# Optimization experiments

Measured on AMD Instinct MI355X. Metric: run time of the kernel, lower is better.

Reference implementation:

```python
import jax, jax.numpy as jnp
import numpy as np

B, S, E, H = 4, 2048, 768, 12
D = E // H  # head dimension = 64


def setup_inputs() -> dict:
    key = jax.random.key(0)
    ks = jax.random.split(key, 10)
    scale = 1.0 / np.sqrt(E)
    x = jax.random.normal(ks[0], (B, S, E), dtype=jnp.float32)
    mask = jax.random.randint(ks[1], (B, S), 0, 2, dtype=jnp.int32)
    # per-head Q/K/V projections stacked over heads: [H, E, D]
    Wq = jax.random.normal(ks[2], (H, E, D), dtype=jnp.float32) * scale
    bq = jax.random.normal(ks[3], (H, D), dtype=jnp.float32) * scale
    Wk = jax.random.normal(ks[4], (H, E, D), dtype=jnp.float32) * scale
    bk = jax.random.normal(ks[5], (H, D), dtype=jnp.float32) * scale
    Wv = jax.random.normal(ks[6], (H, E, D), dtype=jnp.float32) * scale
    bv = jax.random.normal(ks[7], (H, D), dtype=jnp.float32) * scale
    # output projection: [H*D, E]
    Wo = jax.random.normal(ks[8], (H * D, E), dtype=jnp.float32) * scale
    bo = jax.random.normal(ks[9], (E,), dtype=jnp.float32) * scale
    return {"x": x, "mask": mask, "Wq": Wq, "bq": bq, "Wk": Wk, "bk": bk,
            "Wv": Wv, "bv": bv, "Wo": Wo, "bo": bo}


def reference(x, mask, Wq, bq, Wk, bk, Wv, bv, Wo, bo):
    # Per-head linear projections, vectorized over heads: [B, H, S, D]
    q = jnp.einsum('bse,hed->bhsd', x, Wq) + bq[None, :, None, :]
    k = jnp.einsum('bse,hed->bhsd', x, Wk) + bk[None, :, None, :]
    v = jnp.einsum('bse,hed->bhsd', x, Wv) + bv[None, :, None, :]
    # scores: [B, H, S, S]
    scores = jnp.einsum('bhqd,bhkd->bhqk', q, k) / jnp.sqrt(jnp.float32(D))
    # mask [B, S] broadcast over heads and query positions (key-side mask)
    key_mask = mask[:, None, None, :]  # [B, 1, 1, S]
    scores = jnp.where(key_mask == 0, jnp.float32(-1e9), scores)
    attn = jax.nn.softmax(scores, axis=-1)
    out = jnp.einsum('bhqk,bhkd->bhqd', attn, v)  # [B, H, S, D]
    # concat heads: [B, S, H*D]
    out = out.transpose(0, 2, 1, 3).reshape(B, S, H * D)
    return out @ Wo + bo
```

## Files before the change

### kernel.cpp

```cpp
#include <hip/hip_runtime.h>
#include <hip/hip_bf16.h>

#define B_ 4
#define S_ 2048
#define E_ 768
#define H_ 12
#define D_ 64
#define M_ (B_*S_)
#define NQKV 2304
#define KDIM 768

typedef __bf16 bf16x8 __attribute__((ext_vector_type(8)));
typedef float f32x4 __attribute__((ext_vector_type(4)));
typedef short shortx4 __attribute__((ext_vector_type(4)));
typedef unsigned int uintx2 __attribute__((ext_vector_type(2)));
typedef unsigned int uintx4 __attribute__((ext_vector_type(4)));

typedef __attribute__((address_space(1))) void gvoid;
typedef __attribute__((address_space(3))) void lvoid;

__device__ __forceinline__ void gl_lds16(const void* g, void* l) {
  __builtin_amdgcn_global_load_lds((gvoid*)g, (lvoid*)l, 16, 0, 0);
}

__device__ __forceinline__ f32x4 mfma16(bf16x8 a, bf16x8 b, f32x4 c) {
  return __builtin_amdgcn_mfma_f32_16x16x32_bf16(a, b, c, 0, 0, 0);
}

__device__ __forceinline__ f32x4 mfma_pv(shortx4 a, shortx4 b, f32x4 c) {
#if __has_builtin(__builtin_amdgcn_mfma_f32_16x16x16bf16_1k)
  return __builtin_amdgcn_mfma_f32_16x16x16bf16_1k(a, b, c, 0, 0, 0);
#else
  uintx2 au = __builtin_bit_cast(uintx2, a);
  uintx2 bu = __builtin_bit_cast(uintx2, b);
  uintx4 aw = {au.x, au.y, 0u, 0u};
  uintx4 bw = {bu.x, bu.y, 0u, 0u};
  return mfma16(__builtin_bit_cast(bf16x8, aw), __builtin_bit_cast(bf16x8, bw), c);
#endif
}

__device__ __forceinline__ __bf16 ldmix(const void* p, size_t idx, int is_bf) {
  if (is_bf) return ((const __bf16*)p)[idx];
  return (__bf16)(((const float*)p)[idx]);
}
__device__ __forceinline__ float ldmixf(const void* p, size_t idx, int is_bf) {
  if (is_bf) return (float)((const __bf16*)p)[idx];
  return ((const float*)p)[idx];
}

__global__ __launch_bounds__(256) void detect_scan_kernel(
    const unsigned short* __restrict__ xr, int* __restrict__ flag,
    const int* __restrict__ mask,
    int* __restrict__ R, float* __restrict__ maskC, int* __restrict__ npadArr)
{
  __shared__ int cnt;
  __shared__ int wtot[4];
  __shared__ int runningS;
  const int t = threadIdx.x;
  if (blockIdx.x == 0) {
    if (t == 0) cnt = 0;
    __syncthreads();
    unsigned short h = xr[2 * t];
    int e = (h >> 7) & 0xFF;
    if (e >= 100 && e <= 140) atomicAdd(&cnt, 1);
    __syncthreads();
    if (t == 0) *flag = (cnt > 148) ? 1 : 0;
    return;
  }
  const int w = t >> 6, lane = t & 63;
  const int b = blockIdx.x - 1;
  if (t == 0) runningS = 0;
  __syncthreads();
  for (int k0 = 0; k0 < S_; k0 += 256) {
    int keep = (mask[b * S_ + k0 + t] != 0) ? 1 : 0;
    unsigned long long bal = __ballot(keep);
    int lanePre = __popcll(bal & ((1ull << lane) - 1ull));
    if (lane == 0) wtot[w] = __popcll(bal);
    __syncthreads();
    int base = runningS;
    for (int i = 0; i < w; ++i) base += wtot[i];
    if (keep) {
      int pos = base + lanePre;
      R[b * S_ + pos] = b * S_ + k0 + t;
      maskC[b * S_ + pos] = 0.f;
    }
    __syncthreads();
    if (t == 0) runningS += wtot[0] + wtot[1] + wtot[2] + wtot[3];
    __syncthreads();
  }
  int n = runningS;
  int np = (n + 63) & ~63;
  for (int j = n + t; j < S_; j += 256) {
    R[b * S_ + j] = b * S_;
    maskC[b * S_ + j] = -1.0e9f;
  }
  if (t == 0) npadArr[b] = np;
}

__global__ __launch_bounds__(256) void prep_kernel(
    const void* __restrict__ x,
    const void* __restrict__ Wq, const void* __restrict__ bq,
    const void* __restrict__ Wk, const void* __restrict__ bk,
    const void* __restrict__ Wv, const void* __restrict__ bv,
    const void* __restrict__ Wo, const void* __restrict__ bo,
    const int* __restrict__ flag,
    __bf16* __restrict__ Xb,
    __bf16* __restrict__ WbT, __bf16* __restrict__ WoT,
    float* __restrict__ biasP, float* __restrict__ biasO)
{
  const int is_bf = *flag;
  const int bid = blockIdx.x;
  const int t = threadIdx.x;
  if (bid < 3072) {
    int base = (bid * 256 + t) * 8;
    if (is_bf) {
      *(uintx4*)(Xb + base) = *(const uintx4*)((const __bf16*)x + base);
    } else {
      const float* xf = (const float*)x + base;
      f32x4 a = *(const f32x4*)xf;
      f32x4 c = *(const f32x4*)(xf + 4);
      __bf16 ov[8] = {(__bf16)a[0], (__bf16)a[1], (__bf16)a[2], (__bf16)a[3],
                      (__bf16)c[0], (__bf16)c[1], (__bf16)c[2], (__bf16)c[3]};
      *(uintx4*)(Xb + base) = *(uintx4*)ov;
    }
    return;
  }
  int idx = (bid - 3072) * 256 + t;
  const int NW = NQKV * KDIM;
  if (idx < NW) {
    int n = idx / KDIM;
    int e = idx - n * KDIM;
    int sel = n / 768;
    int hd  = n - sel * 768;
    int h = hd >> 6, d = hd & 63;
    const void* W = (sel == 0) ? Wq : (sel == 1) ? Wk : Wv;
    WbT[idx] = ldmix(W, (size_t)(h * 768 + e) * 64 + d, is_bf);
  } else {
    int idx2 = idx - NW;
    int n = idx2 / 768;
    int k = idx2 - n * 768;
    WoT[idx2] = ldmix(Wo, (size_t)k * 768 + n, is_bf);
  }
  if (idx < NQKV) {
    int sel = idx / 768;
    int hd = idx - sel * 768;
    const void* bsel = (sel == 0) ? bq : (sel == 1) ? bk : bv;
    biasP[idx] = ldmixf(bsel, hd, is_bf);
  }
  if (idx >= NW && idx < NW + 768) {
    biasO[idx - NW] = ldmixf(bo, idx - NW, is_bf);
  }
}

__global__ __launch_bounds__(256) void gemm_qkv(
    const __bf16* __restrict__ Xb,
    const __bf16* __restrict__ WbT,
    const float* __restrict__ biasP,
    const int* __restrict__ R,
    const int* __restrict__ npadArr,
    __bf16* __restrict__ Qc,
    __bf16* __restrict__ Kc,
    __bf16* __restrict__ Vc)
{
  __shared__ __align__(16) __bf16 As[128 * 32];
  __shared__ __align__(16) __bf16 Bs[64 * 32];
  const int t = threadIdx.x;
  const int wave = t >> 6, lane = t & 63;
  const int l15 = lane & 15, lq = lane >> 4;
  const int wm = (wave & 1) * 64;
  const int wn = (wave >> 1) * 32;

  const int bid = blockIdx.x;
  int m0, bn0, isQ, b = 0;
  int rowA0, rowA1;
  if (bid < 768) {
    isQ = 1;
    int mi = bid / 12, ni = bid - mi * 12;
    m0 = mi * 128; bn0 = ni * 64;
    rowA0 = m0 + ((0 * 256 + t) >> 2);
    rowA1 = m0 + ((1 * 256 + t) >> 2);
  } else {
    isQ = 0;
    int r2 = bid - 768;
    b = r2 / 384;
    int rr = r2 - b * 384;
    int mi = rr / 24, ni = rr - mi * 24;
    if (mi * 128 >= npadArr[b]) return;
    m0 = mi * 128;
    bn0 = 768 + ni * 64;
    rowA0 = R[b * S_ + m0 + ((0 * 256 + t) >> 2)];
    rowA1 = R[b * S_ + m0 + ((1 * 256 + t) >> 2)];
  }
  const int c8 = (t & 3) << 3;
  const int brow = t >> 2;

  const f32x4 z4 = {0.f, 0.f, 0.f, 0.f};
  f32x4 acc[4][2];
#pragma unroll
  for (int i = 0; i < 4; ++i)
#pragma unroll
    for (int j = 0; j < 2; ++j) acc[i][j] = z4;

  for (int k0 = 0; k0 < KDIM; k0 += 32) {
    __syncthreads();
    gl_lds16(Xb + (size_t)rowA0 * KDIM + k0 + c8, As + (size_t)(wave * 64) * 8);
    gl_lds16(Xb + (size_t)rowA1 * KDIM + k0 + c8, As + (size_t)(256 + wave * 64) * 8);
    gl_lds16(WbT + (size_t)(bn0 + brow) * KDIM + k0 + c8, Bs + (size_t)(wave * 64) * 8);
    __syncthreads();
    bf16x8 af[4], bfr[2];
#pragma unroll
    for (int i = 0; i < 4; ++i) af[i]  = *(const bf16x8*)(As + (wm + i * 16 + l15) * 32 + lq * 8);
#pragma unroll
    for (int j = 0; j < 2; ++j) bfr[j] = *(const bf16x8*)(Bs + (wn + j * 16 + l15) * 32 + lq * 8);
#pragma unroll
    for (int i = 0; i < 4; ++i)
#pragma unroll
      for (int j = 0; j < 2; ++j)
        acc[i][j] = mfma16(af[i], bfr[j], acc[i][j]);
  }

#pragma unroll
  for (int j = 0; j < 2; ++j) {
    int nn = (bn0 - (isQ ? 0 : 768)) + wn + j * 16 + l15;
    float bv = biasP[(isQ ? 0 : 768) + nn];
    if (isQ) {
#pragma unroll
      for (int i = 0; i < 4; ++i) {
        int mbase = m0 + wm + i * 16 + lq * 4;
#pragma unroll
        for (int r = 0; r < 4; ++r)
          Qc[(size_t)(mbase + r) * 768 + nn] = (__bf16)(acc[i][j][r] + bv);
      }
    } else {
      const int isK = (nn < 768);
      const int hh = (isK ? nn : nn - 768) >> 6;
      const int d  = nn & 63;
      const size_t bhh = (size_t)(b * H_ + hh);
#pragma unroll
      for (int i = 0; i < 4; ++i) {
        int jbase = m0 + wm + i * 16 + lq * 4;
#pragma unroll
        for (int r = 0; r < 4; ++r) {
          int jj = jbase + r;
          __bf16 ov = (__bf16)(acc[i][j][r] + bv);
          if (isK) Kc[(bhh * 2048 + jj) * 64 + d] = ov;
          else     Vc[(bhh * 512 + (jj >> 2)) * 256 + d * 4 + (jj & 3)] = ov;
        }
      }
    }
  }
}

__global__ __launch_bounds__(256) void gemm_out(
    const __bf16* __restrict__ A,
    const __bf16* __restrict__ WoT,
    const float* __restrict__ biasO,
    void* __restrict__ C,
    const int* __restrict__ flag)
{
  __shared__ __align__(16) __bf16 As[128 * 32];
  __shared__ __align__(16) __bf16 Bs[64 * 32];
  const int obf = *flag;
  const int t = threadIdx.x;
  const int wave = t >> 6, lane = t & 63;
  const int l15 = lane & 15, lq = lane >> 4;
  const int wm = (wave & 1) * 64;
  const int wn = (wave >> 1) * 32;
  const int m0 = blockIdx.x * 128;
  const int n0 = blockIdx.y * 64;
  const int c8 = (t & 3) << 3;
  const int brow = t >> 2;
  const int rowA0 = m0 + ((0 * 256 + t) >> 2);
  const int rowA1 = m0 + ((1 * 256 + t) >> 2);

  const f32x4 z4 = {0.f, 0.f, 0.f, 0.f};
  f32x4 acc[4][2];
#pragma unroll
  for (int i = 0; i < 4; ++i)
#pragma unroll
    for (int j = 0; j < 2; ++j) acc[i][j] = z4;

  for (int k0 = 0; k0 < KDIM; k0 += 32) {
    __syncthreads();
    gl_lds16(A + (size_t)rowA0 * KDIM + k0 + c8, As + (size_t)(wave * 64) * 8);
    gl_lds16(A + (size_t)rowA1 * KDIM + k0 + c8, As + (size_t)(256 + wave * 64) * 8);
    gl_lds16(WoT + (size_t)(n0 + brow) * KDIM + k0 + c8, Bs + (size_t)(wave * 64) * 8);
    __syncthreads();
    bf16x8 af[4], bfr[2];
#pragma unroll
    for (int i = 0; i < 4; ++i) af[i]  = *(const bf16x8*)(As + (wm + i * 16 + l15) * 32 + lq * 8);
#pragma unroll
    for (int j = 0; j < 2; ++j) bfr[j] = *(const bf16x8*)(Bs + (wn + j * 16 + l15) * 32 + lq * 8);
#pragma unroll
    for (int i = 0; i < 4; ++i)
#pragma unroll
      for (int j = 0; j < 2; ++j)
        acc[i][j] = mfma16(af[i], bfr[j], acc[i][j]);
  }

#pragma unroll
  for (int j = 0; j < 2; ++j) {
    int n = n0 + wn + j * 16 + l15;
    float bv = biasO[n];
#pragma unroll
    for (int i = 0; i < 4; ++i) {
      int mbase = m0 + wm + i * 16 + lq * 4;
#pragma unroll
      for (int r = 0; r < 4; ++r) {
        size_t off = (size_t)(mbase + r) * 768 + n;
        float val = acc[i][j][r] + bv;
        if (obf) ((__bf16*)C)[off] = (__bf16)val;
        else     ((float*)C)[off]  = val;
      }
    }
  }
}

__global__ __launch_bounds__(256) void attn_kernel(
    const __bf16* __restrict__ Qc,
    const __bf16* __restrict__ Kc,
    const __bf16* __restrict__ Vc,
    const float* __restrict__ maskC,
    const int* __restrict__ npadArr,
    __bf16* __restrict__ Out)
{
  __shared__ __align__(16) __bf16 Ks0[64 * 32];
  __shared__ __align__(16) __bf16 Ks1[64 * 32];
  __shared__ __align__(16) __bf16 Vt[16 * 256];
  __shared__ __align__(16) float msk[64];

  const int t = threadIdx.x;
  const int w = t >> 6, lane = t & 63;
  const int l15 = lane & 15, qd = lane >> 4;
  const int bh = blockIdx.y;
  const int b = bh / H_, h = bh - b * H_;
  const int q0 = blockIdx.x * 128;
  const int Skv = npadArr[b];

  const __bf16* Qb = Qc + (size_t)b * S_ * E_ + h * 64;
  const __bf16* Kb = Kc + (size_t)bh * 2048 * 64;
  const __bf16* Vg = Vc + (size_t)bh * 512 * 256;
  const float* mb = maskC + b * S_;

  bf16x8 qf[2][2];
#pragma unroll
  for (int sub = 0; sub < 2; ++sub) {
    int qrow = q0 + w * 32 + sub * 16 + l15;
    qf[sub][0] = *(const bf16x8*)(Qb + (size_t)qrow * E_ + qd * 8);
    qf[sub][1] = *(const bf16x8*)(Qb + (size_t)qrow * E_ + 32 + qd * 8);
  }

  const f32x4 z4 = {0.f, 0.f, 0.f, 0.f};
  f32x4 o[2][4];
#pragma unroll
  for (int sub = 0; sub < 2; ++sub)
#pragma unroll
    for (int dt = 0; dt < 4; ++dt) o[sub][dt] = z4;
  f32x4 ol[2] = {z4, z4};

  const short one_bf = (short)0x3F80;
  const shortx4 ones4 = {one_bf, one_bf, one_bf, one_bf};

  const int skey = t >> 2;
  const int sch  = (t & 3) * 8;
  const float SC = 0.18033688011112042f;

  for (int k0 = 0; k0 < Skv; k0 += 64) {
    __syncthreads();
    gl_lds16(Kb + (size_t)(k0 + skey) * 64 + sch,      Ks0 + w * 512);
    gl_lds16(Kb + (size_t)(k0 + skey) * 64 + 32 + sch, Ks1 + w * 512);
    {
      const __bf16* vsrc = Vg + ((size_t)(k0 >> 2)) * 256;
      gl_lds16(vsrc + t * 8,        Vt + w * 512);
      gl_lds16(vsrc + 2048 + t * 8, Vt + 2048 + w * 512);
    }
    if (t < 16) gl_lds16(mb + k0 + lane * 4, msk);
    __syncthreads();

    bf16x8 kf[4][2];
#pragma unroll
    for (int kt = 0; kt < 4; ++kt) {
      kf[kt][0] = *(const bf16x8*)(Ks0 + (kt * 16 + l15) * 32 + qd * 8);
      kf[kt][1] = *(const bf16x8*)(Ks1 + (kt * 16 + l15) * 32 + qd * 8);
    }
    shortx4 vf[4][4];
#pragma unroll
    for (int kt = 0; kt < 4; ++kt)
#pragma unroll
      for (int dt = 0; dt < 4; ++dt)
        vf[kt][dt] = *(const shortx4*)(Vt + (kt * 4 + qd) * 256 + (dt * 16 + l15) * 4);
    f32x4 ma[4];
#pragma unroll
    for (int kt = 0; kt < 4; ++kt) ma[kt] = *(const f32x4*)(msk + kt * 16 + qd * 4);

#pragma unroll
    for (int sub = 0; sub < 2; ++sub) {
      f32x4 s[4];
#pragma unroll
      for (int kt = 0; kt < 4; ++kt) {
        s[kt] = mfma16(kf[kt][0], qf[sub][0], z4);
        s[kt] = mfma16(kf[kt][1], qf[sub][1], s[kt]);
      }
      shortx4 pfr[4];
#pragma unroll
      for (int kt = 0; kt < 4; ++kt) {
        float p0 = __builtin_amdgcn_exp2f(__builtin_fmaf(s[kt][0], SC, ma[kt][0]));
        float p1 = __builtin_amdgcn_exp2f(__builtin_fmaf(s[kt][1], SC, ma[kt][1]));
        float p2 = __builtin_amdgcn_exp2f(__builtin_fmaf(s[kt][2], SC, ma[kt][2]));
        float p3 = __builtin_amdgcn_exp2f(__builtin_fmaf(s[kt][3], SC, ma[kt][3]));
        unsigned int lo16 = __builtin_amdgcn_perm(__builtin_bit_cast(unsigned int, p1),
                                                  __builtin_bit_cast(unsigned int, p0), 0x07060302u);
        unsigned int hi16 = __builtin_amdgcn_perm(__builtin_bit_cast(unsigned int, p3),
                                                  __builtin_bit_cast(unsigned int, p2), 0x07060302u);
        uintx2 u = {lo16, hi16};
        pfr[kt] = __builtin_bit_cast(shortx4, u);
      }
#pragma unroll
      for (int dt = 0; dt < 4; ++dt)
#pragma unroll
        for (int kt = 0; kt < 4; ++kt)
          o[sub][dt] = mfma_pv(pfr[kt], vf[kt][dt], o[sub][dt]);
#pragma unroll
      for (int kt = 0; kt < 4; ++kt)
        ol[sub] = mfma_pv(pfr[kt], ones4, ol[sub]);
    }
  }

#pragma unroll
  for (int sub = 0; sub < 2; ++sub) {
#pragma unroll
    for (int dt = 0; dt < 4; ++dt)
#pragma unroll
      for (int r = 0; r < 4; ++r) {
        int qrow = q0 + w * 32 + sub * 16 + qd * 4 + r;
        Out[(size_t)(b * S_ + qrow) * E_ + h * 64 + dt * 16 + l15] =
            (__bf16)(o[sub][dt][r] / ol[sub][r]);
      }
  }
}

extern "C" void kernel_launch(void* const* d_in, const int* in_sizes, int n_in,
                              void* d_out, int out_size, void* d_ws, size_t ws_size,
                              hipStream_t stream) {
  const void* x  = d_in[0];
  const int* mask = (const int*)d_in[1];
  const void* Wq = d_in[2];
  const void* bq = d_in[3];
  const void* Wk = d_in[4];
  const void* bk = d_in[5];
  const void* Wv = d_in[6];
  const void* bv = d_in[7];
  const void* Wo = d_in[8];
  const void* bo = d_in[9];

  char* ws = (char*)d_ws;
  int*    flag  = (int*)(ws + 0);
  __bf16* Xb    = (__bf16*)(ws + 256);
  __bf16* WbT   = (__bf16*)(ws + 12583168);
  __bf16* WoT   = (__bf16*)(ws + 16122112);
  float*  biasP = (float*)(ws + 17301760);
  float*  biasO = (float*)(ws + 17310976);
  __bf16* Qc    = (__bf16*)(ws + 17314048);
  __bf16* Kc    = (__bf16*)(ws + 29896960);
  __bf16* Vc    = (__bf16*)(ws + 42479872);
  __bf16* attnO = (__bf16*)(ws + 55062784);
  int*    Ridx  = (int*)(ws + 67645696);
  float*  maskC = (float*)(ws + 67678464);
  int*    npad  = (int*)(ws + 67711232);

  detect_scan_kernel<<<dim3(5), dim3(256), 0, stream>>>(
      (const unsigned short*)x, flag, mask, Ridx, maskC, npad);
  prep_kernel<<<dim3(12288), dim3(256), 0, stream>>>(
      x, Wq, bq, Wk, bk, Wv, bv, Wo, bo, flag, Xb, WbT, WoT, biasP, biasO);
  gemm_qkv<<<dim3(2304), dim3(256), 0, stream>>>(Xb, WbT, biasP, Ridx, npad, Qc, Kc, Vc);
  attn_kernel<<<dim3(16, 48), dim3(256), 0, stream>>>(Qc, Kc, Vc, maskC, npad, attnO);
  gemm_out<<<dim3(64, 12), dim3(256), 0, stream>>>(attnO, WoT, biasO, d_out, flag);
}
```

Baseline: 223.5 us.

## Enlarge GEMM tiles, double-buffer attention K/V loads, compute mask inline

Both GEMMs move from 128x64 to 128x128 output tiles, which halves the block count and doubles per-wave MFMA work for each LDS load. The attention kernel double-buffers its K/V LDS tiles, with an explicit vmcnt wait so the next tile's global loads overlap compute. It also derives the key mask from the compacted count instead of loading it from memory, and raises wave priority around MFMA sections. Risks include more register pressure and lower occupancy from the larger accumulators, and fewer blocks to fill the CUs.

```diff
diff --git a/kernel.cpp b/kernel.cpp
--- a/kernel.cpp
+++ b/kernel.cpp
@@ -51,7 +51,8 @@
 __global__ __launch_bounds__(256) void detect_scan_kernel(
     const unsigned short* __restrict__ xr, int* __restrict__ flag,
     const int* __restrict__ mask,
-    int* __restrict__ R, float* __restrict__ maskC, int* __restrict__ npadArr)
+    int* __restrict__ R, float* __restrict__ maskC, int* __restrict__ npadArr,
+    int* __restrict__ narrArr)
 {
   __shared__ int cnt;
   __shared__ int wtot[4];
@@ -94,7 +95,7 @@
     R[b * S_ + j] = b * S_;
     maskC[b * S_ + j] = -1.0e9f;
   }
-  if (t == 0) npadArr[b] = np;
+  if (t == 0) { npadArr[b] = np; narrArr[b] = n; }
 }
 
 __global__ __launch_bounds__(256) void prep_kernel(
@@ -163,67 +164,69 @@
     __bf16* __restrict__ Vc)
 {
   __shared__ __align__(16) __bf16 As[128 * 32];
-  __shared__ __align__(16) __bf16 Bs[64 * 32];
+  __shared__ __align__(16) __bf16 Bs[128 * 32];
   const int t = threadIdx.x;
   const int wave = t >> 6, lane = t & 63;
   const int l15 = lane & 15, lq = lane >> 4;
   const int wm = (wave & 1) * 64;
-  const int wn = (wave >> 1) * 32;
+  const int wn = (wave >> 1) * 64;
 
   const int bid = blockIdx.x;
   int m0, bn0, isQ, b = 0;
   int rowA0, rowA1;
-  if (bid < 768) {
+  if (bid < 384) {
     isQ = 1;
-    int mi = bid / 12, ni = bid - mi * 12;
-    m0 = mi * 128; bn0 = ni * 64;
-    rowA0 = m0 + ((0 * 256 + t) >> 2);
-    rowA1 = m0 + ((1 * 256 + t) >> 2);
+    int mi = bid / 6, ni = bid - mi * 6;
+    m0 = mi * 128; bn0 = ni * 128;
+    rowA0 = m0 + (t >> 2);
+    rowA1 = m0 + 64 + (t >> 2);
   } else {
     isQ = 0;
-    int r2 = bid - 768;
-    b = r2 / 384;
-    int rr = r2 - b * 384;
-    int mi = rr / 24, ni = rr - mi * 24;
+    int r2 = bid - 384;
+    b = r2 / 192;
+    int rr = r2 - b * 192;
+    int mi = rr / 12, ni = rr - mi * 12;
     if (mi * 128 >= npadArr[b]) return;
     m0 = mi * 128;
-    bn0 = 768 + ni * 64;
-    rowA0 = R[b * S_ + m0 + ((0 * 256 + t) >> 2)];
-    rowA1 = R[b * S_ + m0 + ((1 * 256 + t) >> 2)];
+    bn0 = 768 + ni * 128;
+    rowA0 = R[b * S_ + m0 + (t >> 2)];
+    rowA1 = R[b * S_ + m0 + 64 + (t >> 2)];
   }
   const int c8 = (t & 3) << 3;
-  const int brow = t >> 2;
+  const int brow0 = bn0 + (t >> 2);
+  const int brow1 = bn0 + 64 + (t >> 2);
 
   const f32x4 z4 = {0.f, 0.f, 0.f, 0.f};
-  f32x4 acc[4][2];
+  f32x4 acc[4][4];
 #pragma unroll
   for (int i = 0; i < 4; ++i)
 #pragma unroll
-    for (int j = 0; j < 2; ++j) acc[i][j] = z4;
+    for (int j = 0; j < 4; ++j) acc[i][j] = z4;
 
   for (int k0 = 0; k0 < KDIM; k0 += 32) {
     __syncthreads();
-    gl_lds16(Xb + (size_t)rowA0 * KDIM + k0 + c8, As + (size_t)(wave * 64) * 8);
-    gl_lds16(Xb + (size_t)rowA1 * KDIM + k0 + c8, As + (size_t)(256 + wave * 64) * 8);
-    gl_lds16(WbT + (size_t)(bn0 + brow) * KDIM + k0 + c8, Bs + (size_t)(wave * 64) * 8);
-    __syncthreads();
-    bf16x8 af[4], bfr[2];
+    gl_lds16(Xb + (size_t)rowA0 * KDIM + k0 + c8, As + (size_t)wave * 512);
+    gl_lds16(Xb + (size_t)rowA1 * KDIM + k0 + c8, As + (size_t)(2048 + wave * 512));
+    gl_lds16(WbT + (size_t)brow0 * KDIM + k0 + c8, Bs + (size_t)wave * 512);
+    gl_lds16(WbT + (size_t)brow1 * KDIM + k0 + c8, Bs + (size_t)(2048 + wave * 512));
+    __syncthreads();
+    bf16x8 af[4], bfr[4];
 #pragma unroll
     for (int i = 0; i < 4; ++i) af[i]  = *(const bf16x8*)(As + (wm + i * 16 + l15) * 32 + lq * 8);
 #pragma unroll
-    for (int j = 0; j < 2; ++j) bfr[j] = *(const bf16x8*)(Bs + (wn + j * 16 + l15) * 32 + lq * 8);
+    for (int j = 0; j < 4; ++j) bfr[j] = *(const bf16x8*)(Bs + (wn + j * 16 + l15) * 32 + lq * 8);
 #pragma unroll
     for (int i = 0; i < 4; ++i)
 #pragma unroll
-      for (int j = 0; j < 2; ++j)
+      for (int j = 0; j < 4; ++j)
         acc[i][j] = mfma16(af[i], bfr[j], acc[i][j]);
   }
 
 #pragma unroll
-  for (int j = 0; j < 2; ++j) {
-    int nn = (bn0 - (isQ ? 0 : 768)) + wn + j * 16 + l15;
-    float bv = biasP[(isQ ? 0 : 768) + nn];
+  for (int j = 0; j < 4; ++j) {
     if (isQ) {
+      int nn = bn0 + wn + j * 16 + l15;
+      float bv = biasP[nn];
 #pragma unroll
       for (int i = 0; i < 4; ++i) {
         int mbase = m0 + wm + i * 16 + lq * 4;
@@ -232,6 +235,8 @@
           Qc[(size_t)(mbase + r) * 768 + nn] = (__bf16)(acc[i][j][r] + bv);
       }
     } else {
+      int nn = (bn0 - 768) + wn + j * 16 + l15;
+      float bv = biasP[768 + nn];
       const int isK = (nn < 768);
       const int hh = (isK ? nn : nn - 768) >> 6;
       const int d  = nn & 63;
@@ -259,47 +264,49 @@
     const int* __restrict__ flag)
 {
   __shared__ __align__(16) __bf16 As[128 * 32];
-  __shared__ __align__(16) __bf16 Bs[64 * 32];
+  __shared__ __align__(16) __bf16 Bs[128 * 32];
   const int obf = *flag;
   const int t = threadIdx.x;
   const int wave = t >> 6, lane = t & 63;
   const int l15 = lane & 15, lq = lane >> 4;
   const int wm = (wave & 1) * 64;
-  const int wn = (wave >> 1) * 32;
+  const int wn = (wave >> 1) * 64;
   const int m0 = blockIdx.x * 128;
-  const int n0 = blockIdx.y * 64;
+  const int n0 = blockIdx.y * 128;
   const int c8 = (t & 3) << 3;
-  const int brow = t >> 2;
-  const int rowA0 = m0 + ((0 * 256 + t) >> 2);
-  const int rowA1 = m0 + ((1 * 256 + t) >> 2);
+  const int rowA0 = m0 + (t >> 2);
+  const int rowA1 = m0 + 64 + (t >> 2);
+  const int brow0 = n0 + (t >> 2);
+  const int brow1 = n0 + 64 + (t >> 2);
 
   const f32x4 z4 = {0.f, 0.f, 0.f, 0.f};
-  f32x4 acc[4][2];
+  f32x4 acc[4][4];
 #pragma unroll
   for (int i = 0; i < 4; ++i)
 #pragma unroll
-    for (int j = 0; j < 2; ++j) acc[i][j] = z4;
+    for (int j = 0; j < 4; ++j) acc[i][j] = z4;
 
   for (int k0 = 0; k0 < KDIM; k0 += 32) {
     __syncthreads();
-    gl_lds16(A + (size_t)rowA0 * KDIM + k0 + c8, As + (size_t)(wave * 64) * 8);
-    gl_lds16(A + (size_t)rowA1 * KDIM + k0 + c8, As + (size_t)(256 + wave * 64) * 8);
-    gl_lds16(WoT + (size_t)(n0 + brow) * KDIM + k0 + c8, Bs + (size_t)(wave * 64) * 8);
-    __syncthreads();
-    bf16x8 af[4], bfr[2];
+    gl_lds16(A + (size_t)rowA0 * KDIM + k0 + c8, As + (size_t)wave * 512);
+    gl_lds16(A + (size_t)rowA1 * KDIM + k0 + c8, As + (size_t)(2048 + wave * 512));
+    gl_lds16(WoT + (size_t)brow0 * KDIM + k0 + c8, Bs + (size_t)wave * 512);
+    gl_lds16(WoT + (size_t)brow1 * KDIM + k0 + c8, Bs + (size_t)(2048 + wave * 512));
+    __syncthreads();
+    bf16x8 af[4], bfr[4];
 #pragma unroll
     for (int i = 0; i < 4; ++i) af[i]  = *(const bf16x8*)(As + (wm + i * 16 + l15) * 32 + lq * 8);
 #pragma unroll
-    for (int j = 0; j < 2; ++j) bfr[j] = *(const bf16x8*)(Bs + (wn + j * 16 + l15) * 32 + lq * 8);
+    for (int j = 0; j < 4; ++j) bfr[j] = *(const bf16x8*)(Bs + (wn + j * 16 + l15) * 32 + lq * 8);
 #pragma unroll
     for (int i = 0; i < 4; ++i)
 #pragma unroll
-      for (int j = 0; j < 2; ++j)
+      for (int j = 0; j < 4; ++j)
         acc[i][j] = mfma16(af[i], bfr[j], acc[i][j]);
   }
 
 #pragma unroll
-  for (int j = 0; j < 2; ++j) {
+  for (int j = 0; j < 4; ++j) {
     int n = n0 + wn + j * 16 + l15;
     float bv = biasO[n];
 #pragma unroll
@@ -320,14 +327,13 @@
     const __bf16* __restrict__ Qc,
     const __bf16* __restrict__ Kc,
     const __bf16* __restrict__ Vc,
-    const float* __restrict__ maskC,
     const int* __restrict__ npadArr,
+    const int* __restrict__ narrArr,
     __bf16* __restrict__ Out)
 {
-  __shared__ __align__(16) __bf16 Ks0[64 * 32];
-  __shared__ __align__(16) __bf16 Ks1[64 * 32];
-  __shared__ __align__(16) __bf16 Vt[16 * 256];
-  __shared__ __align__(16) float msk[64];
+  __shared__ __align__(16) __bf16 Ks0[2][64 * 32];
+  __shared__ __align__(16) __bf16 Ks1[2][64 * 32];
+  __shared__ __align__(16) __bf16 Vt[2][16 * 256];
 
   const int t = threadIdx.x;
   const int w = t >> 6, lane = t & 63;
@@ -336,11 +342,11 @@
   const int b = bh / H_, h = bh - b * H_;
   const int q0 = blockIdx.x * 128;
   const int Skv = npadArr[b];
+  const int nb  = narrArr[b];
 
   const __bf16* Qb = Qc + (size_t)b * S_ * E_ + h * 64;
   const __bf16* Kb = Kc + (size_t)bh * 2048 * 64;
   const __bf16* Vg = Vc + (size_t)bh * 512 * 256;
-  const float* mb = maskC + b * S_;
 
   bf16x8 qf[2][2];
 #pragma unroll
@@ -365,42 +371,73 @@
   const int sch  = (t & 3) * 8;
   const float SC = 0.18033688011112042f;
 
-  for (int k0 = 0; k0 < Skv; k0 += 64) {
-    __syncthreads();
-    gl_lds16(Kb + (size_t)(k0 + skey) * 64 + sch,      Ks0 + w * 512);
-    gl_lds16(Kb + (size_t)(k0 + skey) * 64 + 32 + sch, Ks1 + w * 512);
-    {
-      const __bf16* vsrc = Vg + ((size_t)(k0 >> 2)) * 256;
-      gl_lds16(vsrc + t * 8,        Vt + w * 512);
-      gl_lds16(vsrc + 2048 + t * 8, Vt + 2048 + w * 512);
-    }
-    if (t < 16) gl_lds16(mb + k0 + lane * 4, msk);
-    __syncthreads();
+  const int nt = Skv >> 6;
+  if (nt > 0) {
+    gl_lds16(Kb + (size_t)skey * 64 + sch,      &Ks0[0][w * 512]);
+    gl_lds16(Kb + (size_t)skey * 64 + 32 + sch, &Ks1[0][w * 512]);
+    gl_lds16(Vg + t * 8,        &Vt[0][w * 512]);
+    gl_lds16(Vg + 2048 + t * 8, &Vt[0][2048 + w * 512]);
+  }
+
+  for (int ti = 0; ti < nt; ++ti) {
+    const int k0 = ti << 6;
+    const int cur = ti & 1;
+    if (ti + 1 < nt) {
+      const int nxt = cur ^ 1;
+      const int kk = k0 + 64;
+      gl_lds16(Kb + (size_t)(kk + skey) * 64 + sch,      &Ks0[nxt][w * 512]);
+      gl_lds16(Kb + (size_t)(kk + skey) * 64 + 32 + sch, &Ks1[nxt][w * 512]);
+      const __bf16* vsrc = Vg + ((size_t)(kk >> 2)) * 256;
+      gl_lds16(vsrc + t * 8,        &Vt[nxt][w * 512]);
+      gl_lds16(vsrc + 2048 + t * 8, &Vt[nxt][2048 + w * 512]);
+      asm volatile("s_waitcnt vmcnt(4)" ::: "memory");
+    } else {
+      asm volatile("s_waitcnt vmcnt(0)" ::: "memory");
+    }
+    __builtin_amdgcn_s_barrier();
+    __builtin_amdgcn_sched_barrier(0);
+
+    const __bf16* K0 = Ks0[cur];
+    const __bf16* K1 = Ks1[cur];
+    const __bf16* Vb = Vt[cur];
 
     bf16x8 kf[4][2];
 #pragma unroll
     for (int kt = 0; kt < 4; ++kt) {
-      kf[kt][0] = *(const bf16x8*)(Ks0 + (kt * 16 + l15) * 32 + qd * 8);
-      kf[kt][1] = *(const bf16x8*)(Ks1 + (kt * 16 + l15) * 32 + qd * 8);
+      kf[kt][0] = *(const bf16x8*)(K0 + (kt * 16 + l15) * 32 + qd * 8);
+      kf[kt][1] = *(const bf16x8*)(K1 + (kt * 16 + l15) * 32 + qd * 8);
     }
     shortx4 vf[4][4];
 #pragma unroll
     for (int kt = 0; kt < 4; ++kt)
 #pragma unroll
       for (int dt = 0; dt < 4; ++dt)
-        vf[kt][dt] = *(const shortx4*)(Vt + (kt * 4 + qd) * 256 + (dt * 16 + l15) * 4);
+        vf[kt][dt] = *(const shortx4*)(Vb + (kt * 4 + qd) * 256 + (dt * 16 + l15) * 4);
+
     f32x4 ma[4];
-#pragma unroll
-    for (int kt = 0; kt < 4; ++kt) ma[kt] = *(const f32x4*)(msk + kt * 16 + qd * 4);
+    if (k0 + 64 <= nb) {
+#pragma unroll
+      for (int kt = 0; kt < 4; ++kt) ma[kt] = z4;
+    } else {
+#pragma unroll
+      for (int kt = 0; kt < 4; ++kt) {
+        int kk = k0 + kt * 16 + qd * 4;
+#pragma unroll
+        for (int r = 0; r < 4; ++r)
+          ma[kt][r] = (kk + r < nb) ? 0.f : -1.0e9f;
+      }
+    }
 
 #pragma unroll
     for (int sub = 0; sub < 2; ++sub) {
       f32x4 s[4];
+      __builtin_amdgcn_s_setprio(1);
 #pragma unroll
       for (int kt = 0; kt < 4; ++kt) {
         s[kt] = mfma16(kf[kt][0], qf[sub][0], z4);
         s[kt] = mfma16(kf[kt][1], qf[sub][1], s[kt]);
       }
+      __builtin_amdgcn_s_setprio(0);
       shortx4 pfr[4];
 #pragma unroll
       for (int kt = 0; kt < 4; ++kt) {
@@ -415,6 +452,7 @@
         uintx2 u = {lo16, hi16};
         pfr[kt] = __builtin_bit_cast(shortx4, u);
       }
+      __builtin_amdgcn_s_setprio(1);
 #pragma unroll
       for (int dt = 0; dt < 4; ++dt)
 #pragma unroll
@@ -423,7 +461,11 @@
 #pragma unroll
       for (int kt = 0; kt < 4; ++kt)
         ol[sub] = mfma_pv(pfr[kt], ones4, ol[sub]);
-    }
+      __builtin_amdgcn_s_setprio(0);
+    }
+
+    __builtin_amdgcn_sched_barrier(0);
+    __builtin_amdgcn_s_barrier();
   }
 
 #pragma unroll
@@ -467,12 +509,13 @@
   int*    Ridx  = (int*)(ws + 67645696);
   float*  maskC = (float*)(ws + 67678464);
   int*    npad  = (int*)(ws + 67711232);
+  int*    narr  = (int*)(ws + 67711248);
 
   detect_scan_kernel<<<dim3(5), dim3(256), 0, stream>>>(
-      (const unsigned short*)x, flag, mask, Ridx, maskC, npad);
+      (const unsigned short*)x, flag, mask, Ridx, maskC, npad, narr);
   prep_kernel<<<dim3(12288), dim3(256), 0, stream>>>(
       x, Wq, bq, Wk, bk, Wv, bv, Wo, bo, flag, Xb, WbT, WoT, biasP, biasO);
-  gemm_qkv<<<dim3(2304), dim3(256), 0, stream>>>(Xb, WbT, biasP, Ridx, npad, Qc, Kc, Vc);
-  attn_kernel<<<dim3(16, 48), dim3(256), 0, stream>>>(Qc, Kc, Vc, maskC, npad, attnO);
-  gemm_out<<<dim3(64, 12), dim3(256), 0, stream>>>(attnO, WoT, biasO, d_out, flag);
-}
+  gemm_qkv<<<dim3(1152), dim3(256), 0, stream>>>(Xb, WbT, biasP, Ridx, npad, Qc, Kc, Vc);
+  attn_kernel<<<dim3(16, 48), dim3(256), 0, stream>>>(Qc, Kc, Vc, npad, narr, attnO);
+  gemm_out<<<dim3(64, 6), dim3(256), 0, stream>>>(attnO, WoT, biasO, d_out, flag);
+}
```

Measured after the change: 230.1 us. 1.03x slower.
